# Optimization experiments

Measured on AMD Instinct MI355X. Metric: run time of the kernel, lower is better.

The kernel has to match this reference:

```python
import jax, jax.numpy as jnp
import numpy as np
from math import sqrt

DIM = 256
HEADS = 4
GROUPS = min(DIM // 4, 32)  # = 32
EPS = 1e-6


def setup_inputs() -> dict:
    key = jax.random.key(0)
    ks = jax.random.split(key, 10)
    B, C, H, W = 16, DIM, 32, 32
    x = jax.random.normal(ks[0], (B, C, H, W), dtype=jnp.float32)
    s = 1.0 / sqrt(C)
    inp = {
        'x': x,
        'gn_scale': jnp.ones((C,), jnp.float32),
        'gn_bias': jnp.zeros((C,), jnp.float32),
        'Wq': jax.random.normal(ks[1], (C, C), jnp.float32) * s,
        'bq': jnp.zeros((C,), jnp.float32),
        'Wk': jax.random.normal(ks[2], (C, C), jnp.float32) * s,
        'bk': jnp.zeros((C,), jnp.float32),
        'Wv': jax.random.normal(ks[3], (C, C), jnp.float32) * s,
        'bv': jnp.zeros((C,), jnp.float32),
        'Wp': jax.random.normal(ks[4], (C, C), jnp.float32) * s,
        'bp': jnp.zeros((C,), jnp.float32),
    }
    return inp


def _group_norm(x, scale, bias):
    B, C, H, W = x.shape
    xg = x.reshape(B, GROUPS, C // GROUPS, H, W)
    mean = xg.mean(axis=(2, 3, 4), keepdims=True)
    var = xg.var(axis=(2, 3, 4), keepdims=True)
    xg = (xg - mean) * jax.lax.rsqrt(var + EPS)
    x = xg.reshape(B, C, H, W)
    return x * scale[None, :, None, None] + bias[None, :, None, None]


def _lin_ch(x, W, b):
    # 1x1 conv / linear over channel dim: (B,C,H,W) x (C,Cout) -> (B,Cout,H,W)
    return jnp.einsum('bchw,cd->bdhw', x, W) + b[None, :, None, None]


def reference(x, gn_scale, gn_bias, Wq, bq, Wk, bk, Wv, bv, Wp, bp):
    B, C, H, W = x.shape
    dh = C // HEADS
    _x = _group_norm(x, gn_scale, gn_bias)
    q = _lin_ch(_x, Wq, bq).reshape(B, HEADS, dh, H, W)
    k = _lin_ch(_x, Wk, bk).reshape(B, HEADS, dh, H, W)
    v = _lin_ch(_x, Wv, bv).reshape(B, HEADS, dh, H, W)
    scores = jnp.einsum('bhdxy,bhdij->bhxyij', q, k) / sqrt(C)
    scores = scores.reshape(B, HEADS, H, W, H * W)
    weights = jax.nn.softmax(scores, axis=-1).reshape(B, HEADS, H, W, H, W)
    h = jnp.einsum('bhxyij,bhdij->bhdxy', weights, v).reshape(B, C, H, W)
    h = _lin_ch(h, Wp, bp)
    ret = (x + h) / sqrt(2.0)
    return ret
```

## Files before the change

kernel.cpp:

```cpp
#include <hip/hip_runtime.h>
#include <hip/hip_bf16.h>

#define BATCH 16
#define CH    256
#define HW    1024
#define NH    4
#define DH    64
#define NG    32
#define CPG   8
#define EPSV  1e-6f

#define QSCALE 0.090168440055558706f

typedef __bf16 bf16x8 __attribute__((ext_vector_type(8)));
typedef float  f32x4  __attribute__((ext_vector_type(4)));

__device__ __forceinline__ unsigned short f2bf(float f) {
    union { __hip_bfloat16 h; unsigned short u; } cv;
    cv.h = __float2bfloat16(f);
    return cv.u;
}

__device__ __forceinline__ unsigned int fbits(float f) {
    union { float f; unsigned int u; } cv; cv.f = f; return cv.u;
}

__device__ __forceinline__ void gld_lds16(const unsigned short* g, unsigned short* l) {
    __builtin_amdgcn_global_load_lds(
        (const __attribute__((address_space(1))) void*)g,
        (__attribute__((address_space(3))) void*)l, 16, 0, 0);
}

__global__ void prep_gn_kernel(const float* Wq, const float* Wk, const float* Wv,
                               const float* Wp, const float* bq, const float* bk,
                               const float* bv, unsigned short* wqkv_t,
                               unsigned short* wp_t, float* bqkv,
                               const float* x, const float* scale, const float* bias,
                               float* coefA, float* coefB) {
    int t = threadIdx.x;
    if (blockIdx.x < 1024) {
        int idx = blockIdx.x * 256 + t;
        if (idx < 768 * 256) {
            int n = idx >> 8, c = idx & 255;
            const float* W = (n < 256) ? Wq : (n < 512) ? Wk : Wv;
            int d = n & 255;
            wqkv_t[idx] = f2bf(W[c * 256 + d]);
        } else {
            int j = idx - 768 * 256;
            int n = j >> 8, c = j & 255;
            wp_t[j] = f2bf(Wp[c * 256 + n]);
        }
        if (idx < 768)
            bqkv[idx] = (idx < 256) ? bq[idx] : (idx < 512) ? bk[idx - 256] : bv[idx - 512];
    } else {
        int bg = blockIdx.x - 1024;
        const float4* p = reinterpret_cast<const float4*>(x + (size_t)bg * (CPG * HW));
        float s = 0.f, ss = 0.f;
        for (int i = t; i < CPG * HW / 4; i += 256) {
            float4 v = p[i];
            s += v.x + v.y + v.z + v.w;
            ss += v.x * v.x + v.y * v.y + v.z * v.z + v.w * v.w;
        }
        for (int o = 32; o; o >>= 1) { s += __shfl_down(s, o); ss += __shfl_down(ss, o); }
        __shared__ float as_[4], ass_[4];
        int w = t >> 6;
        if ((t & 63) == 0) { as_[w] = s; ass_[w] = ss; }
        __syncthreads();
        if (t < 8) {
            float S = as_[0] + as_[1] + as_[2] + as_[3];
            float SS = ass_[0] + ass_[1] + ass_[2] + ass_[3];
            float mean = S / (float)(CPG * HW);
            float var = SS / (float)(CPG * HW) - mean * mean;
            float rstd = rsqrtf(var + EPSV);
            int b = bg >> 5, g = bg & 31;
            int c = g * CPG + t;
            float a = rstd * scale[c];
            coefA[b * CH + c] = a;
            coefB[b * CH + c] = bias[c] - mean * a;
        }
    }
}

__global__ __launch_bounds__(256, 3) void qkv_kernel(const float* x,
        const float* coefA, const float* coefB,
        const unsigned short* wqkv_t, const float* bqkv,
        unsigned short* qb, unsigned short* kb, unsigned short* vb) {
    int t = threadIdx.x;
    int wv = t >> 6, lane = t & 63, quad = lane >> 4, ln = lane & 15;
    int wr = wv >> 1, wc = wv & 1;
    int bx = blockIdx.x;
    int m0 = bx * 64 + wr * 32;
    int n0 = blockIdx.y * 256 + wc * 128;
    int bb = bx >> 4;
    int p0 = (bx & 15) * 64;

    __shared__ __align__(16) unsigned short lds_a[64][40];

    const float* xb = x + (size_t)bb * CH * HW + p0;
    const float* cA = coefA + bb * CH;
    const float* cB = coefB + bb * CH;

    int sp = t & 63;
    int slot = t >> 6;

    float xv[8];
#pragma unroll
    for (int j = 0; j < 8; j++)
        xv[j] = xb[(size_t)(slot * 8 + j) * HW + sp];

    f32x4 acc[2][8] = {};
    for (int k0 = 0; k0 < CH; k0 += 32) {
        int cb = k0 + slot * 8;
        union { bf16x8 v8; __hip_bfloat162 h2[4]; } u;
#pragma unroll
        for (int j = 0; j < 4; j++) {
            float v0 = fmaf(xv[2 * j],     cA[cb + 2 * j],     cB[cb + 2 * j]);
            float v1 = fmaf(xv[2 * j + 1], cA[cb + 2 * j + 1], cB[cb + 2 * j + 1]);
            u.h2[j] = __float22bfloat162_rn(float2{v0, v1});
        }
        if (k0 + 32 < CH) {
#pragma unroll
            for (int j = 0; j < 8; j++)
                xv[j] = xb[(size_t)(cb + 32 + j) * HW + sp];
        }
        bf16x8 bfr[8];
#pragma unroll
        for (int j = 0; j < 8; j++)
            bfr[j] = *reinterpret_cast<const bf16x8*>(
                wqkv_t + (size_t)(n0 + j * 16 + ln) * CH + k0 + quad * 8);
        __syncthreads();
        int phys = slot ^ (sp & 3);
        *reinterpret_cast<bf16x8*>(&lds_a[sp][phys * 8]) = u.v8;
        __syncthreads();
        bf16x8 af[2];
#pragma unroll
        for (int i = 0; i < 2; i++) {
            int p = wr * 32 + i * 16 + ln;
            af[i] = *reinterpret_cast<const bf16x8*>(&lds_a[p][(quad ^ (p & 3)) * 8]);
        }
#pragma unroll
        for (int i = 0; i < 2; i++)
#pragma unroll
            for (int j = 0; j < 8; j++)
                acc[i][j] = __builtin_amdgcn_mfma_f32_16x16x32_bf16(af[i], bfr[j], acc[i][j], 0, 0, 0);
    }
#pragma unroll
    for (int j = 0; j < 8; j++) {
        int n = n0 + j * 16 + ln;
        float bias = bqkv[n];
        int which = n >> 8;
        int dh_ = n & 255;
        int head = dh_ >> 6, d = dh_ & 63;
#pragma unroll
        for (int i = 0; i < 2; i++) {
            int mb = m0 + i * 16 + quad * 4;
            int bi = mb >> 10, p = mb & 1023;
            int bh = bi * NH + head;
            if (which < 2) {
                unsigned short* dst = (which == 0 ? qb : kb) + (size_t)bh * HW * DH;
                float sc = (which == 0) ? QSCALE : 1.0f;
#pragma unroll
                for (int r = 0; r < 4; r++)
                    dst[(size_t)(p + r) * DH + d] = f2bf((acc[i][j][r] + bias) * sc);
            } else {
                unsigned short* dst = vb + ((size_t)bh * DH + d) * HW + p;
                ushort4 pk4;
                pk4.x = f2bf(acc[i][j][0] + bias);
                pk4.y = f2bf(acc[i][j][1] + bias);
                pk4.z = f2bf(acc[i][j][2] + bias);
                pk4.w = f2bf(acc[i][j][3] + bias);
                *reinterpret_cast<ushort4*>(dst) = pk4;
            }
        }
    }
}

__global__ __launch_bounds__(256) void attn_kernel(const unsigned short* qb,
        const unsigned short* kb, const unsigned short* vb, unsigned short* h_t) {
    int qblk = blockIdx.x, bh = blockIdx.y;
    int t = threadIdx.x;
    int wv = t >> 6, lane = t & 63, quad = lane >> 4, ln = lane & 15;
    int q0 = qblk * 128 + wv * 32;

    const unsigned short* Q = qb + (size_t)bh * HW * DH;
    const unsigned short* K = kb + (size_t)bh * HW * DH;
    const unsigned short* V = vb + (size_t)bh * DH * HW;

    __shared__ __align__(16) unsigned short kbuf[2][4096];
    __shared__ __align__(16) unsigned short vbuf[2][4096];
    __shared__ __align__(16) unsigned short pbuf[4][2][16][72];

    int c_a = wv * 64 + lane;
    int c_b = 256 + wv * 64 + lane;
    int pa = c_a >> 3, ja = (c_a & 7) ^ (pa & 7);
    int pb = c_b >> 3, jb = (c_b & 7) ^ (pb & 7);
    const unsigned short* pka = K + (size_t)pa * DH + ja * 8;
    const unsigned short* pkb = K + (size_t)pb * DH + jb * 8;
    const unsigned short* pva = V + (size_t)pa * HW + ja * 8;
    const unsigned short* pvb = V + (size_t)pb * HW + jb * 8;
    int lofs_a = wv * 512, lofs_b = 2048 + wv * 512;

    int koffs[4][2];
#pragma unroll
    for (int mt = 0; mt < 4; mt++) {
        int p = mt * 16 + ln, sw = p & 7;
#pragma unroll
        for (int kk = 0; kk < 2; kk++)
            koffs[mt][kk] = p * 64 + (((kk * 4 + quad) ^ sw) * 8);
    }

    bf16x8 qf[2][2];
#pragma unroll
    for (int nq = 0; nq < 2; nq++)
#pragma unroll
        for (int kk = 0; kk < 2; kk++)
            qf[nq][kk] = *reinterpret_cast<const bf16x8*>(
                Q + (size_t)(q0 + nq * 16 + ln) * DH + kk * 32 + quad * 8);

    f32x4 ls[2] = {};
    f32x4 o[2][4] = {};

    gld_lds16(pka, &kbuf[0][lofs_a]);
    gld_lds16(pkb, &kbuf[0][lofs_b]);
    gld_lds16(pva, &vbuf[0][lofs_a]);
    gld_lds16(pvb, &vbuf[0][lofs_b]);
    pka += 64 * DH; pkb += 64 * DH; pva += 64; pvb += 64;

#define ATTN_TILE(B, DO_STAGE)                                                      \
    {                                                                               \
        __syncthreads();                                                            \
        if (DO_STAGE) {                                                             \
            gld_lds16(pka, &kbuf[B ^ 1][lofs_a]);                                   \
            gld_lds16(pkb, &kbuf[B ^ 1][lofs_b]);                                   \
            gld_lds16(pva, &vbuf[B ^ 1][lofs_a]);                                   \
            gld_lds16(pvb, &vbuf[B ^ 1][lofs_b]);                                   \
            pka += 64 * DH; pkb += 64 * DH; pva += 64; pvb += 64;                   \
        }                                                                           \
        bf16x8 kf[4][2], vf[4][2];                                                  \
        _Pragma("unroll")                                                           \
        for (int mt = 0; mt < 4; mt++) {                                            \
            _Pragma("unroll")                                                       \
            for (int kk = 0; kk < 2; kk++) {                                        \
                kf[mt][kk] = *reinterpret_cast<const bf16x8*>(&kbuf[B][koffs[mt][kk]]); \
                vf[mt][kk] = *reinterpret_cast<const bf16x8*>(&vbuf[B][koffs[mt][kk]]); \
            }                                                                       \
        }                                                                           \
        f32x4 s[2][4] = {};                                                         \
        __builtin_amdgcn_s_setprio(1);                                              \
        _Pragma("unroll")                                                           \
        for (int nq = 0; nq < 2; nq++)                                              \
            _Pragma("unroll")                                                       \
            for (int mt = 0; mt < 4; mt++) {                                        \
                s[nq][mt] = __builtin_amdgcn_mfma_f32_16x16x32_bf16(kf[mt][0], qf[nq][0], s[nq][mt], 0, 0, 0); \
                s[nq][mt] = __builtin_amdgcn_mfma_f32_16x16x32_bf16(kf[mt][1], qf[nq][1], s[nq][mt], 0, 0, 0); \
            }                                                                       \
        __builtin_amdgcn_s_setprio(0);                                              \
        _Pragma("unroll")                                                           \
        for (int nq = 0; nq < 2; nq++)                                              \
            _Pragma("unroll")                                                       \
            for (int mt = 0; mt < 4; mt++) {                                        \
                float e0 = __builtin_amdgcn_exp2f(s[nq][mt][0]);                    \
                float e1 = __builtin_amdgcn_exp2f(s[nq][mt][1]);                    \
                float e2 = __builtin_amdgcn_exp2f(s[nq][mt][2]);                    \
                float e3 = __builtin_amdgcn_exp2f(s[nq][mt][3]);                    \
                ls[nq][0] += e0; ls[nq][1] += e1;                                   \
                ls[nq][2] += e2; ls[nq][3] += e3;                                   \
                uint2 pk2;                                                          \
                pk2.x = __builtin_amdgcn_perm(fbits(e1), fbits(e0), 0x07060302u);   \
                pk2.y = __builtin_amdgcn_perm(fbits(e3), fbits(e2), 0x07060302u);   \
                *reinterpret_cast<uint2*>(&pbuf[wv][nq][ln][mt * 16 + quad * 4]) = pk2; \
            }                                                                       \
        _Pragma("unroll")                                                           \
        for (int nq = 0; nq < 2; nq++)                                              \
            _Pragma("unroll")                                                       \
            for (int kk = 0; kk < 2; kk++) {                                        \
                bf16x8 pf = *reinterpret_cast<const bf16x8*>(&pbuf[wv][nq][ln][kk * 32 + quad * 8]); \
                __builtin_amdgcn_s_setprio(1);                                      \
                _Pragma("unroll")                                                   \
                for (int mt = 0; mt < 4; mt++)                                      \
                    o[nq][mt] = __builtin_amdgcn_mfma_f32_16x16x32_bf16(vf[mt][kk], pf, o[nq][mt], 0, 0, 0); \
                __builtin_amdgcn_s_setprio(0);                                      \
            }                                                                       \
    }

    for (int u = 0; u < 8; u++) {
        ATTN_TILE(0, true)
        ATTN_TILE(1, (u < 7))
    }
#undef ATTN_TILE

    int b_ = bh >> 2, head = bh & 3;
#pragma unroll
    for (int nq = 0; nq < 2; nq++) {
        float lsum = ls[nq][0] + ls[nq][1] + ls[nq][2] + ls[nq][3];
        lsum += __shfl_xor(lsum, 16);
        lsum += __shfl_xor(lsum, 32);
        float inv = 1.0f / lsum;
        unsigned short* dst = h_t + ((size_t)b_ * HW + q0 + nq * 16 + ln) * CH + head * DH;
#pragma unroll
        for (int mt = 0; mt < 4; mt++) {
            ushort4 pk4;
            pk4.x = f2bf(o[nq][mt][0] * inv);
            pk4.y = f2bf(o[nq][mt][1] * inv);
            pk4.z = f2bf(o[nq][mt][2] * inv);
            pk4.w = f2bf(o[nq][mt][3] * inv);
            *reinterpret_cast<ushort4*>(dst + mt * 16 + quad * 4) = pk4;
        }
    }
}

__global__ __launch_bounds__(256) void proj_kernel(const unsigned short* h_t,
        const unsigned short* wp_t, const float* bp, const float* x, float* out) {
    int t = threadIdx.x;
    int wv = t >> 6, lane = t & 63, quad = lane >> 4, ln = lane & 15;
    int wr = wv >> 1, wc = wv & 1;
    int m0 = blockIdx.x * 64 + wr * 32;
    int n0 = blockIdx.y * 128 + wc * 64;

    f32x4 acc[2][4] = {};
    for (int k0 = 0; k0 < CH; k0 += 32) {
        int koff = k0 + quad * 8;
        bf16x8 af[2], bfr[4];
#pragma unroll
        for (int i = 0; i < 2; i++)
            af[i] = *reinterpret_cast<const bf16x8*>(h_t + (size_t)(m0 + i * 16 + ln) * CH + koff);
#pragma unroll
        for (int j = 0; j < 4; j++)
            bfr[j] = *reinterpret_cast<const bf16x8*>(wp_t + (size_t)(n0 + j * 16 + ln) * CH + koff);
#pragma unroll
        for (int i = 0; i < 2; i++)
#pragma unroll
            for (int j = 0; j < 4; j++)
                acc[i][j] = __builtin_amdgcn_mfma_f32_16x16x32_bf16(af[i], bfr[j], acc[i][j], 0, 0, 0);
    }
    const float inv_s2 = 0.70710678118654752440f;
#pragma unroll
    for (int j = 0; j < 4; j++) {
        int n = n0 + j * 16 + ln;
        float bias = bp[n];
#pragma unroll
        for (int i = 0; i < 2; i++) {
            int mb = m0 + i * 16 + quad * 4;
            int bi = mb >> 10, p = mb & 1023;
            size_t off = ((size_t)(bi * CH + n)) * HW + p;
            float4 xv = *reinterpret_cast<const float4*>(x + off);
            float4 ov;
            ov.x = (xv.x + acc[i][j][0] + bias) * inv_s2;
            ov.y = (xv.y + acc[i][j][1] + bias) * inv_s2;
            ov.z = (xv.z + acc[i][j][2] + bias) * inv_s2;
            ov.w = (xv.w + acc[i][j][3] + bias) * inv_s2;
            *reinterpret_cast<float4*>(out + off) = ov;
        }
    }
}

extern "C" void kernel_launch(void* const* d_in, const int* in_sizes, int n_in,
                              void* d_out, int out_size, void* d_ws, size_t ws_size,
                              hipStream_t stream) {
    const float* x        = (const float*)d_in[0];
    const float* gn_scale = (const float*)d_in[1];
    const float* gn_bias  = (const float*)d_in[2];
    const float* Wq = (const float*)d_in[3];
    const float* bq = (const float*)d_in[4];
    const float* Wk = (const float*)d_in[5];
    const float* bk = (const float*)d_in[6];
    const float* Wv = (const float*)d_in[7];
    const float* bv = (const float*)d_in[8];
    const float* Wp = (const float*)d_in[9];
    const float* bp = (const float*)d_in[10];
    float* out = (float*)d_out;

    char* ws = (char*)d_ws;
    float*          bqkv   = (float*)(ws + 0);
    float*          coefA  = (float*)(ws + 4096);
    float*          coefB  = (float*)(ws + 20480);
    unsigned short* wqkv_t = (unsigned short*)(ws + 36864);
    unsigned short* wp_t   = (unsigned short*)(ws + 430080);
    unsigned short* h_t    = (unsigned short*)(ws + 1048576);
    unsigned short* qb     = (unsigned short*)(ws + 9437184);
    unsigned short* kb     = (unsigned short*)(ws + 17825792);
    unsigned short* vb     = (unsigned short*)(ws + 26214400);

    prep_gn_kernel<<<1536, 256, 0, stream>>>(Wq, Wk, Wv, Wp, bq, bk, bv,
                                             wqkv_t, wp_t, bqkv,
                                             x, gn_scale, gn_bias, coefA, coefB);
    qkv_kernel<<<dim3(256, 3), 256, 0, stream>>>(x, coefA, coefB, wqkv_t, bqkv, qb, kb, vb);
    attn_kernel<<<dim3(8, 64), 256, 0, stream>>>(qb, kb, vb, h_t);
    proj_kernel<<<dim3(256, 2), 256, 0, stream>>>(h_t, wp_t, bp, x, out);
}
```

Before: 172.9 us.

## Materialize normalized bf16 activations in GN kernel and simplify QKV GEMM tiling

The group-norm stats kernel now keeps its loaded x values in registers and writes a normalized, transposed bf16 activation buffer (pixel-major, channel-contiguous). The QKV GEMM then reads both operands directly from global memory with 128x128 block tiles and 64x64 per-wave tiles, with no LDS staging and no block barriers. This removes the per-tile fp32 load, normalize and transpose work and the two syncthreads inside the QKV loop, at the cost of an extra 8 MB bf16 write and read. The attention kernel also drops its s_setprio hints around the MFMA blocks.

```diff
diff --git a/kernel.cpp b/kernel.cpp
--- a/kernel.cpp
+++ b/kernel.cpp
@@ -36,7 +36,7 @@
                                const float* bv, unsigned short* wqkv_t,
                                unsigned short* wp_t, float* bqkv,
                                const float* x, const float* scale, const float* bias,
-                               float* coefA, float* coefB) {
+                               unsigned short* xn) {
     int t = threadIdx.x;
     if (blockIdx.x < 1024) {
         int idx = blockIdx.x * 256 + t;
@@ -55,14 +55,18 @@
     } else {
         int bg = blockIdx.x - 1024;
         const float4* p = reinterpret_cast<const float4*>(x + (size_t)bg * (CPG * HW));
+        float va[8][4];
         float s = 0.f, ss = 0.f;
-        for (int i = t; i < CPG * HW / 4; i += 256) {
-            float4 v = p[i];
+#pragma unroll
+        for (int k = 0; k < 8; k++) {
+            float4 v = p[t + 256 * k];
+            va[k][0] = v.x; va[k][1] = v.y; va[k][2] = v.z; va[k][3] = v.w;
             s += v.x + v.y + v.z + v.w;
             ss += v.x * v.x + v.y * v.y + v.z * v.z + v.w * v.w;
         }
         for (int o = 32; o; o >>= 1) { s += __shfl_down(s, o); ss += __shfl_down(ss, o); }
         __shared__ float as_[4], ass_[4];
+        __shared__ float sA[8], sB[8];
         int w = t >> 6;
         if ((t & 63) == 0) { as_[w] = s; ass_[w] = ss; }
         __syncthreads();
@@ -72,87 +76,65 @@
             float mean = S / (float)(CPG * HW);
             float var = SS / (float)(CPG * HW) - mean * mean;
             float rstd = rsqrtf(var + EPSV);
-            int b = bg >> 5, g = bg & 31;
+            int g = bg & 31;
             int c = g * CPG + t;
             float a = rstd * scale[c];
-            coefA[b * CH + c] = a;
-            coefB[b * CH + c] = bias[c] - mean * a;
-        }
-    }
-}
-
-__global__ __launch_bounds__(256, 3) void qkv_kernel(const float* x,
-        const float* coefA, const float* coefB,
+            sA[t] = a;
+            sB[t] = bias[c] - mean * a;
+        }
+        __syncthreads();
+        int b = bg >> 5, g = bg & 31;
+        unsigned short* dst = xn + ((size_t)b * HW + t * 4) * CH + g * CPG;
+#pragma unroll
+        for (int pl = 0; pl < 4; pl++) {
+            union { bf16x8 v8; __hip_bfloat162 h2[4]; } u;
+#pragma unroll
+            for (int c2 = 0; c2 < 4; c2++) {
+                float v0 = fmaf(va[2 * c2][pl],     sA[2 * c2],     sB[2 * c2]);
+                float v1 = fmaf(va[2 * c2 + 1][pl], sA[2 * c2 + 1], sB[2 * c2 + 1]);
+                u.h2[c2] = __float22bfloat162_rn(float2{v0, v1});
+            }
+            *reinterpret_cast<bf16x8*>(dst + (size_t)pl * CH) = u.v8;
+        }
+    }
+}
+
+__global__ __launch_bounds__(256) void qkv_kernel(const unsigned short* xn,
         const unsigned short* wqkv_t, const float* bqkv,
         unsigned short* qb, unsigned short* kb, unsigned short* vb) {
     int t = threadIdx.x;
     int wv = t >> 6, lane = t & 63, quad = lane >> 4, ln = lane & 15;
     int wr = wv >> 1, wc = wv & 1;
-    int bx = blockIdx.x;
-    int m0 = bx * 64 + wr * 32;
-    int n0 = blockIdx.y * 256 + wc * 128;
-    int bb = bx >> 4;
-    int p0 = (bx & 15) * 64;
-
-    __shared__ __align__(16) unsigned short lds_a[64][40];
-
-    const float* xb = x + (size_t)bb * CH * HW + p0;
-    const float* cA = coefA + bb * CH;
-    const float* cB = coefB + bb * CH;
-
-    int sp = t & 63;
-    int slot = t >> 6;
-
-    float xv[8];
-#pragma unroll
-    for (int j = 0; j < 8; j++)
-        xv[j] = xb[(size_t)(slot * 8 + j) * HW + sp];
-
-    f32x4 acc[2][8] = {};
+    int m0 = blockIdx.x * 128 + wr * 64;
+    int n0 = blockIdx.y * 128 + wc * 64;
+
+    f32x4 acc[4][4] = {};
     for (int k0 = 0; k0 < CH; k0 += 32) {
-        int cb = k0 + slot * 8;
-        union { bf16x8 v8; __hip_bfloat162 h2[4]; } u;
-#pragma unroll
-        for (int j = 0; j < 4; j++) {
-            float v0 = fmaf(xv[2 * j],     cA[cb + 2 * j],     cB[cb + 2 * j]);
-            float v1 = fmaf(xv[2 * j + 1], cA[cb + 2 * j + 1], cB[cb + 2 * j + 1]);
-            u.h2[j] = __float22bfloat162_rn(float2{v0, v1});
-        }
-        if (k0 + 32 < CH) {
-#pragma unroll
-            for (int j = 0; j < 8; j++)
-                xv[j] = xb[(size_t)(cb + 32 + j) * HW + sp];
-        }
-        bf16x8 bfr[8];
-#pragma unroll
-        for (int j = 0; j < 8; j++)
+        int koff = k0 + quad * 8;
+        bf16x8 af[4], bfr[4];
+#pragma unroll
+        for (int i = 0; i < 4; i++)
+            af[i] = *reinterpret_cast<const bf16x8*>(
+                xn + (size_t)(m0 + i * 16 + ln) * CH + koff);
+#pragma unroll
+        for (int j = 0; j < 4; j++)
             bfr[j] = *reinterpret_cast<const bf16x8*>(
-                wqkv_t + (size_t)(n0 + j * 16 + ln) * CH + k0 + quad * 8);
-        __syncthreads();
-        int phys = slot ^ (sp & 3);
-        *reinterpret_cast<bf16x8*>(&lds_a[sp][phys * 8]) = u.v8;
-        __syncthreads();
-        bf16x8 af[2];
-#pragma unroll
-        for (int i = 0; i < 2; i++) {
-            int p = wr * 32 + i * 16 + ln;
-            af[i] = *reinterpret_cast<const bf16x8*>(&lds_a[p][(quad ^ (p & 3)) * 8]);
-        }
-#pragma unroll
-        for (int i = 0; i < 2; i++)
-#pragma unroll
-            for (int j = 0; j < 8; j++)
+                wqkv_t + (size_t)(n0 + j * 16 + ln) * CH + koff);
+#pragma unroll
+        for (int i = 0; i < 4; i++)
+#pragma unroll
+            for (int j = 0; j < 4; j++)
                 acc[i][j] = __builtin_amdgcn_mfma_f32_16x16x32_bf16(af[i], bfr[j], acc[i][j], 0, 0, 0);
     }
 #pragma unroll
-    for (int j = 0; j < 8; j++) {
+    for (int j = 0; j < 4; j++) {
         int n = n0 + j * 16 + ln;
         float bias = bqkv[n];
         int which = n >> 8;
         int dh_ = n & 255;
         int head = dh_ >> 6, d = dh_ & 63;
 #pragma unroll
-        for (int i = 0; i < 2; i++) {
+        for (int i = 0; i < 4; i++) {
             int mb = m0 + i * 16 + quad * 4;
             int bi = mb >> 10, p = mb & 1023;
             int bh = bi * NH + head;
@@ -246,7 +228,6 @@
             }                                                                       \
         }                                                                           \
         f32x4 s[2][4] = {};                                                         \
-        __builtin_amdgcn_s_setprio(1);                                              \
         _Pragma("unroll")                                                           \
         for (int nq = 0; nq < 2; nq++)                                              \
             _Pragma("unroll")                                                       \
@@ -254,7 +235,6 @@
                 s[nq][mt] = __builtin_amdgcn_mfma_f32_16x16x32_bf16(kf[mt][0], qf[nq][0], s[nq][mt], 0, 0, 0); \
                 s[nq][mt] = __builtin_amdgcn_mfma_f32_16x16x32_bf16(kf[mt][1], qf[nq][1], s[nq][mt], 0, 0, 0); \
             }                                                                       \
-        __builtin_amdgcn_s_setprio(0);                                              \
         _Pragma("unroll")                                                           \
         for (int nq = 0; nq < 2; nq++)                                              \
             _Pragma("unroll")                                                       \
@@ -275,11 +255,9 @@
             _Pragma("unroll")                                                       \
             for (int kk = 0; kk < 2; kk++) {                                        \
                 bf16x8 pf = *reinterpret_cast<const bf16x8*>(&pbuf[wv][nq][ln][kk * 32 + quad * 8]); \
-                __builtin_amdgcn_s_setprio(1);                                      \
                 _Pragma("unroll")                                                   \
                 for (int mt = 0; mt < 4; mt++)                                      \
                     o[nq][mt] = __builtin_amdgcn_mfma_f32_16x16x32_bf16(vf[mt][kk], pf, o[nq][mt], 0, 0, 0); \
-                __builtin_amdgcn_s_setprio(0);                                      \
             }                                                                       \
     }
 
@@ -372,19 +350,18 @@
 
     char* ws = (char*)d_ws;
     float*          bqkv   = (float*)(ws + 0);
-    float*          coefA  = (float*)(ws + 4096);
-    float*          coefB  = (float*)(ws + 20480);
     unsigned short* wqkv_t = (unsigned short*)(ws + 36864);
     unsigned short* wp_t   = (unsigned short*)(ws + 430080);
-    unsigned short* h_t    = (unsigned short*)(ws + 1048576);
-    unsigned short* qb     = (unsigned short*)(ws + 9437184);
-    unsigned short* kb     = (unsigned short*)(ws + 17825792);
-    unsigned short* vb     = (unsigned short*)(ws + 26214400);
+    unsigned short* xn     = (unsigned short*)(ws + 1048576);
+    unsigned short* h_t    = (unsigned short*)(ws + 9437184);
+    unsigned short* qb     = (unsigned short*)(ws + 17825792);
+    unsigned short* kb     = (unsigned short*)(ws + 26214400);
+    unsigned short* vb     = (unsigned short*)(ws + 34603008);
 
     prep_gn_kernel<<<1536, 256, 0, stream>>>(Wq, Wk, Wv, Wp, bq, bk, bv,
                                              wqkv_t, wp_t, bqkv,
-                                             x, gn_scale, gn_bias, coefA, coefB);
-    qkv_kernel<<<dim3(256, 3), 256, 0, stream>>>(x, coefA, coefB, wqkv_t, bqkv, qb, kb, vb);
+                                             x, gn_scale, gn_bias, xn);
+    qkv_kernel<<<dim3(128, 6), 256, 0, stream>>>(xn, wqkv_t, bqkv, qb, kb, vb);
     attn_kernel<<<dim3(8, 64), 256, 0, stream>>>(qb, kb, vb, h_t);
     proj_kernel<<<dim3(256, 2), 256, 0, stream>>>(h_t, wp_t, bp, x, out);
 }
```

Result: faster. 165.4 us (-4.3%).
